# Kernel tuning notes

Measured on AMD Instinct MI355X. Metric: run time of the kernel, lower is better.

Reference implementation:

```python
import jax, jax.numpy as jnp
import numpy as np

IN_F, OUT_F, MAX_LEN = 768, 512, 1024
NEG_INF = -9e15

def leaky_relu(x, slope=0.2):
    return jnp.where(x >= 0, x, slope * x)

def setup_inputs() -> dict:
    key = jax.random.key(0)
    k1, k2, k3, k4, k5, k6, k7 = jax.random.split(key, 7)
    B, N = 8, 1024
    h = jax.random.normal(k1, (B, N, IN_F), dtype=jnp.float32)
    adj = jax.random.randint(k2, (B, N, N), 0, 2, dtype=jnp.int32)
    positions = jax.random.randint(k3, (B, N), 0, MAX_LEN, dtype=jnp.int64)
    # learned params (nn.Linear stores weight [out,in]; we keep [in,out] for x@W)
    W = jax.random.normal(k4, (IN_F, OUT_F), dtype=jnp.float32) / np.sqrt(IN_F)
    # a: Linear(2*OUT_F, 1) -> vector of length 2*OUT_F, split into a1 (self) / a2 (neighbor)
    a = jax.random.normal(k5, (2 * OUT_F,), dtype=jnp.float32) / np.sqrt(2 * OUT_F)
    pos_table = jax.random.normal(k6, (MAX_LEN, OUT_F), dtype=jnp.float32) * 0.02
    return {"h": h, "adj": adj, "positions": positions, "W": W, "a": a, "pos_table": pos_table}

def reference(h, adj, positions, W, a, pos_table):
    # Wh: [B,N,Do]
    Wh = jnp.einsum("bnd,do->bno", h, W) + pos_table[positions]
    # additive-attention trick: a([Wh_i ; Wh_j]) = Wh_i@a1 + Wh_j@a2
    a1, a2 = a[:OUT_F], a[OUT_F:]
    f1 = Wh @ a1  # [B,N] score contribution of source (repeat_interleave side)
    f2 = Wh @ a2  # [B,N] score contribution of target (repeat side)
    e = leaky_relu(f1[:, :, None] + f2[:, None, :])  # [B,N,N]
    e = jnp.where(adj > 0, e, NEG_INF)
    attention = jax.nn.softmax(e, axis=-1)  # [B,N,N]
    h_prime = jnp.einsum("bnm,bmo->bno", attention, Wh)  # [B,N,Do]
    return h_prime, attention
```

## Files before the change

### kernel.cpp

```cpp
#include <hip/hip_runtime.h>
#include <stdint.h>

#define BATCH 8
#define NNODE 1024
#define INF 768
#define OUTF 512
#define MTOT (BATCH * NNODE)

typedef __attribute__((ext_vector_type(8))) short short8;
typedef __attribute__((ext_vector_type(4))) short short4v;
typedef __attribute__((ext_vector_type(4))) float floatx4;

__device__ __forceinline__ unsigned short f2bf(float f) {
  union { float f; unsigned u; } v; v.f = f;
  unsigned r = v.u + 0x7fffu + ((v.u >> 16) & 1u);
  return (unsigned short)(r >> 16);
}

__device__ __forceinline__ void gload_lds16(const void* g, void* l) {
  __builtin_amdgcn_global_load_lds(
      (const __attribute__((address_space(1))) void*)g,
      (__attribute__((address_space(3))) void*)l, 16, 0, 0);
}

__global__ __launch_bounds__(256) void prep_kernel(
    const float* __restrict__ h, const float* __restrict__ W,
    short* __restrict__ hbf, short* __restrict__ Wt, float* __restrict__ f12) {
  __shared__ float tile[32][33];
  int bid = blockIdx.x;
  int t = threadIdx.x;
  if (bid < 3072) {
    size_t i = ((size_t)bid * 256 + t) * 8;
    float4 v0 = *(const float4*)&h[i];
    float4 v1 = *(const float4*)&h[i + 4];
    short8 o;
    o[0] = (short)f2bf(v0.x); o[1] = (short)f2bf(v0.y);
    o[2] = (short)f2bf(v0.z); o[3] = (short)f2bf(v0.w);
    o[4] = (short)f2bf(v1.x); o[5] = (short)f2bf(v1.y);
    o[6] = (short)f2bf(v1.z); o[7] = (short)f2bf(v1.w);
    *(short8*)&hbf[i] = o;
    if (bid < 16) {
      float4 z = make_float4(0.f, 0.f, 0.f, 0.f);
      *(float4*)&f12[bid * 1024 + t * 4] = z;
    }
  } else {
    int tb = bid - 3072;
    int o0 = (tb & 15) * 32;
    int k0 = (tb >> 4) * 32;
    int x = t & 31, y = t >> 5;
#pragma unroll
    for (int q = 0; q < 4; ++q) {
      int r = y * 4 + q;
      tile[r][x] = W[(size_t)(k0 + r) * OUTF + o0 + x];
    }
    __syncthreads();
#pragma unroll
    for (int q = 0; q < 4; ++q) {
      int r = y * 4 + q;
      Wt[(size_t)(o0 + r) * INF + k0 + x] = (short)f2bf(tile[x][r]);
    }
  }
}

__global__ __launch_bounds__(512) void gemm1_kernel(
    const short* __restrict__ hbf, const short* __restrict__ Wt,
    const int* __restrict__ positions, const float* __restrict__ pos_table,
    const float* __restrict__ a, float* __restrict__ f12,
    short* __restrict__ Wht) {
  __shared__ short smem[4][8192];
  int bid0 = blockIdx.x;
  int bid = (bid0 & 7) * 32 + (bid0 >> 3);
  int nt = bid & 3, mt = bid >> 2;
  int M0 = mt * 128, N0 = nt * 128;
  int t = threadIdx.x;
  int wv = t >> 6, lane = t & 63;
  int wr = (wv >> 2) * 64, wc = (wv & 3) * 32;
  int l16 = lane & 15, kq = lane >> 4;

  floatx4 acc[4][2] = {};

  auto stage = [&](int buf, int kt) {
#pragma unroll
    for (int i = 0; i < 2; ++i) {
      int q = wv * 64 + lane + i * 512;
      int row = q >> 3;
      int cg = (q & 7) ^ (row & 7);
      gload_lds16(&hbf[(size_t)(M0 + row) * INF + kt * 64 + cg * 8],
                  &smem[buf * 2][(wv * 64 + i * 512) * 8]);
      gload_lds16(&Wt[(size_t)(N0 + row) * INF + kt * 64 + cg * 8],
                  &smem[buf * 2 + 1][(wv * 64 + i * 512) * 8]);
    }
  };

  stage(0, 0);
  __syncthreads();
  int cur = 0;
  for (int kt = 0; kt < 12; ++kt) {
    if (kt < 11) stage(cur ^ 1, kt + 1);
    const short* As = smem[cur * 2];
    const short* Bs = smem[cur * 2 + 1];
#pragma unroll
    for (int ks = 0; ks < 2; ++ks) {
      short8 af[4], bfv[2];
#pragma unroll
      for (int mi = 0; mi < 4; ++mi) {
        int r = wr + mi * 16 + l16;
        af[mi] = *(const short8*)&As[r * 64 + (((ks * 4 + kq) ^ (r & 7)) * 8)];
      }
#pragma unroll
      for (int ni = 0; ni < 2; ++ni) {
        int r = wc + ni * 16 + l16;
        bfv[ni] = *(const short8*)&Bs[r * 64 + (((ks * 4 + kq) ^ (r & 7)) * 8)];
      }
#pragma unroll
      for (int mi = 0; mi < 4; ++mi)
#pragma unroll
        for (int ni = 0; ni < 2; ++ni)
          acc[mi][ni] = __builtin_amdgcn_mfma_f32_16x16x32_bf16(af[mi], bfv[ni], acc[mi][ni], 0, 0, 0);
    }
    __syncthreads();
    cur ^= 1;
  }

  int oc0 = N0 + wc + l16;
  int oc1 = oc0 + 16;
#pragma unroll
  for (int mi = 0; mi < 4; ++mi)
#pragma unroll
    for (int j = 0; j < 4; ++j) {
      int row = M0 + wr + mi * 16 + kq * 4 + j;
      int pos = positions[row];
      acc[mi][0][j] += pos_table[(size_t)pos * OUTF + oc0];
      acc[mi][1][j] += pos_table[(size_t)pos * OUTF + oc1];
    }
  short* T = &smem[0][0];
#pragma unroll
  for (int mi = 0; mi < 4; ++mi)
#pragma unroll
    for (int ni = 0; ni < 2; ++ni)
#pragma unroll
      for (int j = 0; j < 4; ++j)
        T[(wc + ni * 16 + l16) * 136 + wr + mi * 16 + kq * 4 + j] =
            (short)f2bf(acc[mi][ni][j]);
  float a10 = a[oc0], a11 = a[oc1];
  float a20 = a[OUTF + oc0], a21 = a[OUTF + oc1];
  float v1[16], v2[16];
#pragma unroll
  for (int mi = 0; mi < 4; ++mi)
#pragma unroll
    for (int j = 0; j < 4; ++j) {
      v1[mi * 4 + j] = acc[mi][0][j] * a10 + acc[mi][1][j] * a11;
      v2[mi * 4 + j] = acc[mi][0][j] * a20 + acc[mi][1][j] * a21;
    }
#pragma unroll
  for (int mlen = 8; mlen >= 1; mlen >>= 1) {
    bool hi = (l16 & mlen) != 0;
#pragma unroll
    for (int i = 0; i < mlen; ++i) {
      float k1 = hi ? v1[mlen + i] : v1[i];
      float s1 = hi ? v1[i] : v1[mlen + i];
      float k2 = hi ? v2[mlen + i] : v2[i];
      float s2 = hi ? v2[i] : v2[mlen + i];
      v1[i] = k1 + __shfl_xor(s1, mlen);
      v2[i] = k2 + __shfl_xor(s2, mlen);
    }
  }
  {
    int rrow = M0 + wr + (l16 >> 2) * 16 + kq * 4 + (l16 & 3);
    atomicAdd(&f12[rrow], v1[0]);
    atomicAdd(&f12[MTOT + rrow], v2[0]);
  }
  __syncthreads();
  int bb = M0 >> 10, i0 = M0 & 1023;
#pragma unroll
  for (int i = 0; i < 4; ++i) {
    int c = t + i * 512;
    int row = c >> 4;
    int mc = (c & 15) * 8;
    short8 vv = *(const short8*)&T[row * 136 + mc];
    *(short8*)&Wht[((size_t)bb * OUTF + N0 + row) * NNODE + i0 + mc] = vv;
  }
}

__global__ __launch_bounds__(256) void softmax_kernel(
    const float* __restrict__ f1, const float* __restrict__ f2,
    const int* __restrict__ adj, float* __restrict__ att,
    short* __restrict__ attbf) {
  int m = blockIdx.x;
  int b = m >> 10;
  int t = threadIdx.x;
  int wave = t >> 6, lane = t & 63;
  __shared__ float red[4];
  float f1v = f1[m];
  int4 av = ((const int4*)(adj + (size_t)m * NNODE))[t];
  float4 fv = ((const float4*)(f2 + b * NNODE))[t];
  float e[4];
  {
    float x;
    x = f1v + fv.x; x = x >= 0.f ? x : 0.2f * x; e[0] = av.x > 0 ? x : -9e15f;
    x = f1v + fv.y; x = x >= 0.f ? x : 0.2f * x; e[1] = av.y > 0 ? x : -9e15f;
    x = f1v + fv.z; x = x >= 0.f ? x : 0.2f * x; e[2] = av.z > 0 ? x : -9e15f;
    x = f1v + fv.w; x = x >= 0.f ? x : 0.2f * x; e[3] = av.w > 0 ? x : -9e15f;
  }
  float mx = fmaxf(fmaxf(e[0], e[1]), fmaxf(e[2], e[3]));
#pragma unroll
  for (int off = 32; off; off >>= 1) mx = fmaxf(mx, __shfl_xor(mx, off));
  if (lane == 0) red[wave] = mx;
  __syncthreads();
  mx = fmaxf(fmaxf(red[0], red[1]), fmaxf(red[2], red[3]));
  __syncthreads();
  float p[4], s = 0.f;
#pragma unroll
  for (int q = 0; q < 4; ++q) { p[q] = expf(e[q] - mx); s += p[q]; }
#pragma unroll
  for (int off = 32; off; off >>= 1) s += __shfl_xor(s, off);
  if (lane == 0) red[wave] = s;
  __syncthreads();
  s = red[0] + red[1] + red[2] + red[3];
  float inv = 1.f / s;
  float4 o = make_float4(p[0] * inv, p[1] * inv, p[2] * inv, p[3] * inv);
  ((float4*)(att + (size_t)m * NNODE))[t] = o;
  short4v ob;
  ob[0] = (short)f2bf(o.x); ob[1] = (short)f2bf(o.y);
  ob[2] = (short)f2bf(o.z); ob[3] = (short)f2bf(o.w);
  ((short4v*)(attbf + (size_t)m * NNODE))[t] = ob;
}

__global__ __launch_bounds__(512) void pv_kernel(
    const short* __restrict__ attbf, const short* __restrict__ Wht,
    float* __restrict__ hp) {
  __shared__ short smem[4][8192];
  int bid0 = blockIdx.x;
  int bid = (bid0 & 7) * 32 + (bid0 >> 3);
  int nt = bid & 3, mt = bid >> 2;
  int M0 = mt * 128, N0 = nt * 128;
  const short* Wb = Wht + (size_t)(M0 >> 10) * OUTF * NNODE;
  int t = threadIdx.x;
  int wv = t >> 6, lane = t & 63;
  int wr = (wv >> 2) * 64, wc = (wv & 3) * 32;
  int l16 = lane & 15, kq = lane >> 4;

  floatx4 acc[4][2] = {};

  auto stage = [&](int buf, int kt) {
#pragma unroll
    for (int i = 0; i < 2; ++i) {
      int q = wv * 64 + lane + i * 512;
      int row = q >> 3;
      int cg = (q & 7) ^ (row & 7);
      gload_lds16(&attbf[(size_t)(M0 + row) * NNODE + kt * 64 + cg * 8],
                  &smem[buf * 2][(wv * 64 + i * 512) * 8]);
      gload_lds16(&Wb[(size_t)(N0 + row) * NNODE + kt * 64 + cg * 8],
                  &smem[buf * 2 + 1][(wv * 64 + i * 512) * 8]);
    }
  };

  stage(0, 0);
  __syncthreads();
  int cur = 0;
  for (int kt = 0; kt < 16; ++kt) {
    if (kt < 15) stage(cur ^ 1, kt + 1);
    const short* As = smem[cur * 2];
    const short* Bs = smem[cur * 2 + 1];
#pragma unroll
    for (int ks = 0; ks < 2; ++ks) {
      short8 af[4], bfv[2];
#pragma unroll
      for (int mi = 0; mi < 4; ++mi) {
        int r = wr + mi * 16 + l16;
        af[mi] = *(const short8*)&As[r * 64 + (((ks * 4 + kq) ^ (r & 7)) * 8)];
      }
#pragma unroll
      for (int ni = 0; ni < 2; ++ni) {
        int r = wc + ni * 16 + l16;
        bfv[ni] = *(const short8*)&Bs[r * 64 + (((ks * 4 + kq) ^ (r & 7)) * 8)];
      }
#pragma unroll
      for (int mi = 0; mi < 4; ++mi)
#pragma unroll
        for (int ni = 0; ni < 2; ++ni)
          acc[mi][ni] = __builtin_amdgcn_mfma_f32_16x16x32_bf16(af[mi], bfv[ni], acc[mi][ni], 0, 0, 0);
    }
    __syncthreads();
    cur ^= 1;
  }

#pragma unroll
  for (int mi = 0; mi < 4; ++mi) {
#pragma unroll
    for (int j = 0; j < 4; ++j) {
      int row = M0 + wr + mi * 16 + kq * 4 + j;
#pragma unroll
      for (int ni = 0; ni < 2; ++ni) {
        int col = N0 + wc + ni * 16 + l16;
        hp[(size_t)row * OUTF + col] = acc[mi][ni][j];
      }
    }
  }
}

extern "C" void kernel_launch(void* const* d_in, const int* in_sizes, int n_in,
                              void* d_out, int out_size, void* d_ws, size_t ws_size,
                              hipStream_t stream) {
  const float* h = (const float*)d_in[0];
  const int* adj = (const int*)d_in[1];
  const int* positions = (const int*)d_in[2];
  const float* W = (const float*)d_in[3];
  const float* a = (const float*)d_in[4];
  const float* pos_table = (const float*)d_in[5];

  float* hp = (float*)d_out;
  float* att = hp + (size_t)MTOT * OUTF;

  char* ws = (char*)d_ws;
  short* Wt = (short*)ws;
  short* Wht = (short*)(ws + 786432);
  float* f12 = (float*)(ws + 786432 + 8388608);
  short* hbf = (short*)(ws + 786432 + 8388608 + 65536);
  short* attbf = hbf;

  prep_kernel<<<3456, 256, 0, stream>>>(h, W, hbf, Wt, f12);
  gemm1_kernel<<<256, 512, 0, stream>>>(hbf, Wt, positions, pos_table, a, f12, Wht);
  softmax_kernel<<<8192, 256, 0, stream>>>(f12, f12 + MTOT, adj, att, attbf);
  pv_kernel<<<256, 512, 0, stream>>>(attbf, Wht, hp);
}
```

Measured before the change: 58.40 us.

## Fuse masked softmax into PV GEMM, keeping bf16 probabilities in LDS

Replaces the separate softmax and PV kernels with one kernel. Each block computes the masked leaky-relu softmax for 32 rows across all 1024 columns, writes the fp32 attention output, and stores the bf16 probabilities in swizzled LDS. It then multiplies them by the full 512-wide Wh tile streamed through double-buffered LDS. This removes the bf16 attention round-trip through global memory and one launch. The cost is only 256 blocks, each holding 64 exp values per thread in registers, and a full pass over Wh per 32 rows.

```diff
diff --git a/kernel.cpp b/kernel.cpp
--- a/kernel.cpp
+++ b/kernel.cpp
@@ -182,121 +182,115 @@
   }
 }
 
-__global__ __launch_bounds__(256) void softmax_kernel(
-    const float* __restrict__ f1, const float* __restrict__ f2,
-    const int* __restrict__ adj, float* __restrict__ att,
-    short* __restrict__ attbf) {
-  int m = blockIdx.x;
-  int b = m >> 10;
-  int t = threadIdx.x;
-  int wave = t >> 6, lane = t & 63;
-  __shared__ float red[4];
-  float f1v = f1[m];
-  int4 av = ((const int4*)(adj + (size_t)m * NNODE))[t];
-  float4 fv = ((const float4*)(f2 + b * NNODE))[t];
-  float e[4];
-  {
-    float x;
-    x = f1v + fv.x; x = x >= 0.f ? x : 0.2f * x; e[0] = av.x > 0 ? x : -9e15f;
-    x = f1v + fv.y; x = x >= 0.f ? x : 0.2f * x; e[1] = av.y > 0 ? x : -9e15f;
-    x = f1v + fv.z; x = x >= 0.f ? x : 0.2f * x; e[2] = av.z > 0 ? x : -9e15f;
-    x = f1v + fv.w; x = x >= 0.f ? x : 0.2f * x; e[3] = av.w > 0 ? x : -9e15f;
-  }
-  float mx = fmaxf(fmaxf(e[0], e[1]), fmaxf(e[2], e[3]));
-#pragma unroll
-  for (int off = 32; off; off >>= 1) mx = fmaxf(mx, __shfl_xor(mx, off));
-  if (lane == 0) red[wave] = mx;
-  __syncthreads();
-  mx = fmaxf(fmaxf(red[0], red[1]), fmaxf(red[2], red[3]));
-  __syncthreads();
-  float p[4], s = 0.f;
-#pragma unroll
-  for (int q = 0; q < 4; ++q) { p[q] = expf(e[q] - mx); s += p[q]; }
-#pragma unroll
-  for (int off = 32; off; off >>= 1) s += __shfl_xor(s, off);
-  if (lane == 0) red[wave] = s;
-  __syncthreads();
-  s = red[0] + red[1] + red[2] + red[3];
-  float inv = 1.f / s;
-  float4 o = make_float4(p[0] * inv, p[1] * inv, p[2] * inv, p[3] * inv);
-  ((float4*)(att + (size_t)m * NNODE))[t] = o;
-  short4v ob;
-  ob[0] = (short)f2bf(o.x); ob[1] = (short)f2bf(o.y);
-  ob[2] = (short)f2bf(o.z); ob[3] = (short)f2bf(o.w);
-  ((short4v*)(attbf + (size_t)m * NNODE))[t] = ob;
-}
-
-__global__ __launch_bounds__(512) void pv_kernel(
-    const short* __restrict__ attbf, const short* __restrict__ Wht,
+__global__ __launch_bounds__(512) void smpv_kernel(
+    const float* __restrict__ f12, const int* __restrict__ adj,
+    const short* __restrict__ Wht, float* __restrict__ att,
     float* __restrict__ hp) {
-  __shared__ short smem[4][8192];
+  __shared__ short lds[65536];
+  short* pbf = lds;
+  short* Bbuf0 = lds + 32768;
+  short* Bbuf1 = lds + 49152;
+
   int bid0 = blockIdx.x;
-  int bid = (bid0 & 7) * 32 + (bid0 >> 3);
-  int nt = bid & 3, mt = bid >> 2;
-  int M0 = mt * 128, N0 = nt * 128;
-  const short* Wb = Wht + (size_t)(M0 >> 10) * OUTF * NNODE;
+  int b = bid0 & 7, rb = bid0 >> 3;
+  int r0 = rb * 32;
   int t = threadIdx.x;
   int wv = t >> 6, lane = t & 63;
-  int wr = (wv >> 2) * 64, wc = (wv & 3) * 32;
   int l16 = lane & 15, kq = lane >> 4;
-
-  floatx4 acc[4][2] = {};
-
-  auto stage = [&](int buf, int kt) {
-#pragma unroll
-    for (int i = 0; i < 2; ++i) {
+  const short* Wb = Wht + (size_t)b * OUTF * NNODE;
+
+  auto stageB = [&](short* dst, int kt) {
+#pragma unroll
+    for (int i = 0; i < 4; ++i) {
       int q = wv * 64 + lane + i * 512;
-      int row = q >> 3;
-      int cg = (q & 7) ^ (row & 7);
-      gload_lds16(&attbf[(size_t)(M0 + row) * NNODE + kt * 64 + cg * 8],
-                  &smem[buf * 2][(wv * 64 + i * 512) * 8]);
-      gload_lds16(&Wb[(size_t)(N0 + row) * NNODE + kt * 64 + cg * 8],
-                  &smem[buf * 2 + 1][(wv * 64 + i * 512) * 8]);
+      int r = q >> 2, s = q & 3;
+      int cg = s ^ (r & 3);
+      gload_lds16(&Wb[(size_t)r * NNODE + kt * 32 + cg * 8],
+                  dst + (wv * 64 + i * 512) * 8);
     }
   };
-
-  stage(0, 0);
+  stageB(Bbuf0, 0);
+
+  {
+    int row = t >> 4, sub = t & 15;
+    int gm = b * NNODE + r0 + row;
+    float f1v = f12[gm];
+    const float* f2b = f12 + MTOT + b * NNODE;
+    const int* adjrow = adj + (size_t)gm * NNODE;
+    float e[64];
+#pragma unroll
+    for (int i = 0; i < 16; ++i) {
+      int col = sub * 4 + i * 64;
+      int4 av = *(const int4*)&adjrow[col];
+      float4 fv = *(const float4*)&f2b[col];
+      float x;
+      x = f1v + fv.x; x = x >= 0.f ? x : 0.2f * x; e[i * 4 + 0] = av.x > 0 ? x : -9e15f;
+      x = f1v + fv.y; x = x >= 0.f ? x : 0.2f * x; e[i * 4 + 1] = av.y > 0 ? x : -9e15f;
+      x = f1v + fv.z; x = x >= 0.f ? x : 0.2f * x; e[i * 4 + 2] = av.z > 0 ? x : -9e15f;
+      x = f1v + fv.w; x = x >= 0.f ? x : 0.2f * x; e[i * 4 + 3] = av.w > 0 ? x : -9e15f;
+    }
+    float mx = e[0];
+#pragma unroll
+    for (int i = 1; i < 64; ++i) mx = fmaxf(mx, e[i]);
+#pragma unroll
+    for (int off = 1; off < 16; off <<= 1) mx = fmaxf(mx, __shfl_xor(mx, off));
+    float s = 0.f;
+#pragma unroll
+    for (int i = 0; i < 64; ++i) { e[i] = expf(e[i] - mx); s += e[i]; }
+#pragma unroll
+    for (int off = 1; off < 16; off <<= 1) s += __shfl_xor(s, off);
+    float inv = 1.f / s;
+    float* attrow = att + (size_t)gm * NNODE;
+#pragma unroll
+    for (int i = 0; i < 16; ++i) {
+      int col = sub * 4 + i * 64;
+      float4 o = make_float4(e[i * 4] * inv, e[i * 4 + 1] * inv,
+                             e[i * 4 + 2] * inv, e[i * 4 + 3] * inv);
+      *(float4*)&attrow[col] = o;
+      int c = (sub >> 1) + 8 * i;
+      short4v pb;
+      pb[0] = (short)f2bf(o.x); pb[1] = (short)f2bf(o.y);
+      pb[2] = (short)f2bf(o.z); pb[3] = (short)f2bf(o.w);
+      *(short4v*)&pbf[row * 1024 + ((c ^ (row & 7)) * 8) + (sub & 1) * 4] = pb;
+    }
+  }
   __syncthreads();
+
+  int wc = wv * 64;
+  floatx4 acc[2][4] = {};
   int cur = 0;
-  for (int kt = 0; kt < 16; ++kt) {
-    if (kt < 15) stage(cur ^ 1, kt + 1);
-    const short* As = smem[cur * 2];
-    const short* Bs = smem[cur * 2 + 1];
-#pragma unroll
-    for (int ks = 0; ks < 2; ++ks) {
-      short8 af[4], bfv[2];
-#pragma unroll
-      for (int mi = 0; mi < 4; ++mi) {
-        int r = wr + mi * 16 + l16;
-        af[mi] = *(const short8*)&As[r * 64 + (((ks * 4 + kq) ^ (r & 7)) * 8)];
-      }
-#pragma unroll
-      for (int ni = 0; ni < 2; ++ni) {
-        int r = wc + ni * 16 + l16;
-        bfv[ni] = *(const short8*)&Bs[r * 64 + (((ks * 4 + kq) ^ (r & 7)) * 8)];
-      }
-#pragma unroll
-      for (int mi = 0; mi < 4; ++mi)
-#pragma unroll
-        for (int ni = 0; ni < 2; ++ni)
-          acc[mi][ni] = __builtin_amdgcn_mfma_f32_16x16x32_bf16(af[mi], bfv[ni], acc[mi][ni], 0, 0, 0);
-    }
+  for (int kt = 0; kt < 32; ++kt) {
+    if (kt < 31) stageB(cur ? Bbuf0 : Bbuf1, kt + 1);
+    const short* Bsc = cur ? Bbuf1 : Bbuf0;
+    short8 af[2], bfv[4];
+#pragma unroll
+    for (int mi = 0; mi < 2; ++mi) {
+      int r = mi * 16 + l16;
+      af[mi] = *(const short8*)&pbf[r * 1024 + (((kt * 4 + kq) ^ (r & 7)) * 8)];
+    }
+#pragma unroll
+    for (int ni = 0; ni < 4; ++ni) {
+      int r = wc + ni * 16 + l16;
+      bfv[ni] = *(const short8*)&Bsc[r * 32 + ((kq ^ (r & 3)) * 8)];
+    }
+#pragma unroll
+    for (int mi = 0; mi < 2; ++mi)
+#pragma unroll
+      for (int ni = 0; ni < 4; ++ni)
+        acc[mi][ni] = __builtin_amdgcn_mfma_f32_16x16x32_bf16(af[mi], bfv[ni], acc[mi][ni], 0, 0, 0);
     __syncthreads();
     cur ^= 1;
   }
 
 #pragma unroll
-  for (int mi = 0; mi < 4; ++mi) {
+  for (int mi = 0; mi < 2; ++mi)
 #pragma unroll
     for (int j = 0; j < 4; ++j) {
-      int row = M0 + wr + mi * 16 + kq * 4 + j;
-#pragma unroll
-      for (int ni = 0; ni < 2; ++ni) {
-        int col = N0 + wc + ni * 16 + l16;
-        hp[(size_t)row * OUTF + col] = acc[mi][ni][j];
-      }
-    }
-  }
+      int grow = b * NNODE + r0 + mi * 16 + kq * 4 + j;
+#pragma unroll
+      for (int ni = 0; ni < 4; ++ni)
+        hp[(size_t)grow * OUTF + wc + ni * 16 + l16] = acc[mi][ni][j];
+    }
 }
 
 extern "C" void kernel_launch(void* const* d_in, const int* in_sizes, int n_in,
@@ -317,10 +311,8 @@
   short* Wht = (short*)(ws + 786432);
   float* f12 = (float*)(ws + 786432 + 8388608);
   short* hbf = (short*)(ws + 786432 + 8388608 + 65536);
-  short* attbf = hbf;
 
   prep_kernel<<<3456, 256, 0, stream>>>(h, W, hbf, Wt, f12);
   gemm1_kernel<<<256, 512, 0, stream>>>(hbf, Wt, positions, pos_table, a, f12, Wht);
-  softmax_kernel<<<8192, 256, 0, stream>>>(f12, f12 + MTOT, adj, att, attbf);
-  pv_kernel<<<256, 512, 0, stream>>>(attbf, Wht, hp);
-}
+  smpv_kernel<<<256, 512, 0, stream>>>(f12, adj, Wht, att, hp);
+}
```

Measured after the change: 68.54 us. +17.4%, slower.

## Use 4-wave 64x64 warp tiles with K-tile 32 in both GEMM kernels

Applied to the files above, without the earlier changes.

Both MFMA GEMM kernels drop from 512 to 256 threads per block. Each wave now computes a 64x64 output tile instead of 64x32, and the LDS K-tile shrinks from 64 to 32 with a matching XOR swizzle. This raises fragment reuse per wave and lowers LDS footprint. The cost is half the waves per CU for latency hiding and twice as many K iterations and barriers.

```diff
diff --git a/kernel.cpp b/kernel.cpp
--- a/kernel.cpp
+++ b/kernel.cpp
@@ -62,95 +62,98 @@
   }
 }
 
-__global__ __launch_bounds__(512) void gemm1_kernel(
+__global__ __launch_bounds__(256) void gemm1_kernel(
     const short* __restrict__ hbf, const short* __restrict__ Wt,
     const int* __restrict__ positions, const float* __restrict__ pos_table,
     const float* __restrict__ a, float* __restrict__ f12,
     short* __restrict__ Wht) {
-  __shared__ short smem[4][8192];
+  __shared__ short smem[20480];
   int bid0 = blockIdx.x;
   int bid = (bid0 & 7) * 32 + (bid0 >> 3);
   int nt = bid & 3, mt = bid >> 2;
   int M0 = mt * 128, N0 = nt * 128;
   int t = threadIdx.x;
   int wv = t >> 6, lane = t & 63;
-  int wr = (wv >> 2) * 64, wc = (wv & 3) * 32;
+  int wr = (wv >> 1) * 64, wc = (wv & 1) * 64;
   int l16 = lane & 15, kq = lane >> 4;
 
-  floatx4 acc[4][2] = {};
+  floatx4 acc[4][4] = {};
 
   auto stage = [&](int buf, int kt) {
 #pragma unroll
     for (int i = 0; i < 2; ++i) {
-      int q = wv * 64 + lane + i * 512;
-      int row = q >> 3;
-      int cg = (q & 7) ^ (row & 7);
-      gload_lds16(&hbf[(size_t)(M0 + row) * INF + kt * 64 + cg * 8],
-                  &smem[buf * 2][(wv * 64 + i * 512) * 8]);
-      gload_lds16(&Wt[(size_t)(N0 + row) * INF + kt * 64 + cg * 8],
-                  &smem[buf * 2 + 1][(wv * 64 + i * 512) * 8]);
+      int q = t + i * 256;
+      int row = q >> 2;
+      int cg = (q & 3) ^ ((row >> 1) & 3);
+      gload_lds16(&hbf[(size_t)(M0 + row) * INF + kt * 32 + cg * 8],
+                  &smem[buf * 4096 + q * 8]);
+      gload_lds16(&Wt[(size_t)(N0 + row) * INF + kt * 32 + cg * 8],
+                  &smem[8192 + buf * 4096 + q * 8]);
     }
   };
 
   stage(0, 0);
   __syncthreads();
-  int cur = 0;
-  for (int kt = 0; kt < 12; ++kt) {
-    if (kt < 11) stage(cur ^ 1, kt + 1);
-    const short* As = smem[cur * 2];
-    const short* Bs = smem[cur * 2 + 1];
-#pragma unroll
-    for (int ks = 0; ks < 2; ++ks) {
-      short8 af[4], bfv[2];
-#pragma unroll
-      for (int mi = 0; mi < 4; ++mi) {
-        int r = wr + mi * 16 + l16;
-        af[mi] = *(const short8*)&As[r * 64 + (((ks * 4 + kq) ^ (r & 7)) * 8)];
-      }
-#pragma unroll
-      for (int ni = 0; ni < 2; ++ni) {
-        int r = wc + ni * 16 + l16;
-        bfv[ni] = *(const short8*)&Bs[r * 64 + (((ks * 4 + kq) ^ (r & 7)) * 8)];
-      }
-#pragma unroll
-      for (int mi = 0; mi < 4; ++mi)
-#pragma unroll
-        for (int ni = 0; ni < 2; ++ni)
-          acc[mi][ni] = __builtin_amdgcn_mfma_f32_16x16x32_bf16(af[mi], bfv[ni], acc[mi][ni], 0, 0, 0);
-    }
+  for (int kt = 0; kt < 24; ++kt) {
+    if (kt < 23) stage((kt + 1) & 1, kt + 1);
+    const short* As = &smem[(kt & 1) * 4096];
+    const short* Bs = &smem[8192 + (kt & 1) * 4096];
+    short8 af[4], bfv[4];
+#pragma unroll
+    for (int mi = 0; mi < 4; ++mi) {
+      int r = wr + mi * 16 + l16;
+      af[mi] = *(const short8*)&As[r * 32 + ((kq ^ ((r >> 1) & 3)) * 8)];
+    }
+#pragma unroll
+    for (int ni = 0; ni < 4; ++ni) {
+      int r = wc + ni * 16 + l16;
+      bfv[ni] = *(const short8*)&Bs[r * 32 + ((kq ^ ((r >> 1) & 3)) * 8)];
+    }
+#pragma unroll
+    for (int mi = 0; mi < 4; ++mi)
+#pragma unroll
+      for (int ni = 0; ni < 4; ++ni)
+        acc[mi][ni] = __builtin_amdgcn_mfma_f32_16x16x32_bf16(af[mi], bfv[ni], acc[mi][ni], 0, 0, 0);
     __syncthreads();
-    cur ^= 1;
-  }
-
-  int oc0 = N0 + wc + l16;
-  int oc1 = oc0 + 16;
+  }
+
+  int oc[4];
+#pragma unroll
+  for (int ni = 0; ni < 4; ++ni) oc[ni] = N0 + wc + ni * 16 + l16;
 #pragma unroll
   for (int mi = 0; mi < 4; ++mi)
 #pragma unroll
     for (int j = 0; j < 4; ++j) {
       int row = M0 + wr + mi * 16 + kq * 4 + j;
       int pos = positions[row];
-      acc[mi][0][j] += pos_table[(size_t)pos * OUTF + oc0];
-      acc[mi][1][j] += pos_table[(size_t)pos * OUTF + oc1];
-    }
-  short* T = &smem[0][0];
+      const float* pt = &pos_table[(size_t)pos * OUTF];
+#pragma unroll
+      for (int ni = 0; ni < 4; ++ni) acc[mi][ni][j] += pt[oc[ni]];
+    }
+  short* T = smem;
 #pragma unroll
   for (int mi = 0; mi < 4; ++mi)
 #pragma unroll
-    for (int ni = 0; ni < 2; ++ni)
+    for (int ni = 0; ni < 4; ++ni)
 #pragma unroll
       for (int j = 0; j < 4; ++j)
         T[(wc + ni * 16 + l16) * 136 + wr + mi * 16 + kq * 4 + j] =
             (short)f2bf(acc[mi][ni][j]);
-  float a10 = a[oc0], a11 = a[oc1];
-  float a20 = a[OUTF + oc0], a21 = a[OUTF + oc1];
+  float a1v[4], a2v[4];
+#pragma unroll
+  for (int ni = 0; ni < 4; ++ni) { a1v[ni] = a[oc[ni]]; a2v[ni] = a[OUTF + oc[ni]]; }
   float v1[16], v2[16];
 #pragma unroll
   for (int mi = 0; mi < 4; ++mi)
 #pragma unroll
     for (int j = 0; j < 4; ++j) {
-      v1[mi * 4 + j] = acc[mi][0][j] * a10 + acc[mi][1][j] * a11;
-      v2[mi * 4 + j] = acc[mi][0][j] * a20 + acc[mi][1][j] * a21;
+      float s1 = 0.f, s2 = 0.f;
+#pragma unroll
+      for (int ni = 0; ni < 4; ++ni) {
+        s1 += acc[mi][ni][j] * a1v[ni];
+        s2 += acc[mi][ni][j] * a2v[ni];
+      }
+      v1[mi * 4 + j] = s1; v2[mi * 4 + j] = s2;
     }
 #pragma unroll
   for (int mlen = 8; mlen >= 1; mlen >>= 1) {
@@ -173,8 +176,8 @@
   __syncthreads();
   int bb = M0 >> 10, i0 = M0 & 1023;
 #pragma unroll
-  for (int i = 0; i < 4; ++i) {
-    int c = t + i * 512;
+  for (int i = 0; i < 8; ++i) {
+    int c = t + i * 256;
     int row = c >> 4;
     int mc = (c & 15) * 8;
     short8 vv = *(const short8*)&T[row * 136 + mc];
@@ -226,10 +229,10 @@
   ((short4v*)(attbf + (size_t)m * NNODE))[t] = ob;
 }
 
-__global__ __launch_bounds__(512) void pv_kernel(
+__global__ __launch_bounds__(256) void pv_kernel(
     const short* __restrict__ attbf, const short* __restrict__ Wht,
     float* __restrict__ hp) {
-  __shared__ short smem[4][8192];
+  __shared__ short smem[16384];
   int bid0 = blockIdx.x;
   int bid = (bid0 & 7) * 32 + (bid0 >> 3);
   int nt = bid & 3, mt = bid >> 2;
@@ -237,66 +240,58 @@
   const short* Wb = Wht + (size_t)(M0 >> 10) * OUTF * NNODE;
   int t = threadIdx.x;
   int wv = t >> 6, lane = t & 63;
-  int wr = (wv >> 2) * 64, wc = (wv & 3) * 32;
+  int wr = (wv >> 1) * 64, wc = (wv & 1) * 64;
   int l16 = lane & 15, kq = lane >> 4;
 
-  floatx4 acc[4][2] = {};
+  floatx4 acc[4][4] = {};
 
   auto stage = [&](int buf, int kt) {
 #pragma unroll
     for (int i = 0; i < 2; ++i) {
-      int q = wv * 64 + lane + i * 512;
-      int row = q >> 3;
-      int cg = (q & 7) ^ (row & 7);
-      gload_lds16(&attbf[(size_t)(M0 + row) * NNODE + kt * 64 + cg * 8],
-                  &smem[buf * 2][(wv * 64 + i * 512) * 8]);
-      gload_lds16(&Wb[(size_t)(N0 + row) * NNODE + kt * 64 + cg * 8],
-                  &smem[buf * 2 + 1][(wv * 64 + i * 512) * 8]);
+      int q = t + i * 256;
+      int row = q >> 2;
+      int cg = (q & 3) ^ ((row >> 1) & 3);
+      gload_lds16(&attbf[(size_t)(M0 + row) * NNODE + kt * 32 + cg * 8],
+                  &smem[buf * 4096 + q * 8]);
+      gload_lds16(&Wb[(size_t)(N0 + row) * NNODE + kt * 32 + cg * 8],
+                  &smem[8192 + buf * 4096 + q * 8]);
     }
   };
 
   stage(0, 0);
   __syncthreads();
-  int cur = 0;
-  for (int kt = 0; kt < 16; ++kt) {
-    if (kt < 15) stage(cur ^ 1, kt + 1);
-    const short* As = smem[cur * 2];
-    const short* Bs = smem[cur * 2 + 1];
-#pragma unroll
-    for (int ks = 0; ks < 2; ++ks) {
-      short8 af[4], bfv[2];
-#pragma unroll
-      for (int mi = 0; mi < 4; ++mi) {
-        int r = wr + mi * 16 + l16;
-        af[mi] = *(const short8*)&As[r * 64 + (((ks * 4 + kq) ^ (r & 7)) * 8)];
-      }
-#pragma unroll
-      for (int ni = 0; ni < 2; ++ni) {
-        int r = wc + ni * 16 + l16;
-        bfv[ni] = *(const short8*)&Bs[r * 64 + (((ks * 4 + kq) ^ (r & 7)) * 8)];
-      }
-#pragma unroll
-      for (int mi = 0; mi < 4; ++mi)
-#pragma unroll
-        for (int ni = 0; ni < 2; ++ni)
-          acc[mi][ni] = __builtin_amdgcn_mfma_f32_16x16x32_bf16(af[mi], bfv[ni], acc[mi][ni], 0, 0, 0);
-    }
+  for (int kt = 0; kt < 32; ++kt) {
+    if (kt < 31) stage((kt + 1) & 1, kt + 1);
+    const short* As = &smem[(kt & 1) * 4096];
+    const short* Bs = &smem[8192 + (kt & 1) * 4096];
+    short8 af[4], bfv[4];
+#pragma unroll
+    for (int mi = 0; mi < 4; ++mi) {
+      int r = wr + mi * 16 + l16;
+      af[mi] = *(const short8*)&As[r * 32 + ((kq ^ ((r >> 1) & 3)) * 8)];
+    }
+#pragma unroll
+    for (int ni = 0; ni < 4; ++ni) {
+      int r = wc + ni * 16 + l16;
+      bfv[ni] = *(const short8*)&Bs[r * 32 + ((kq ^ ((r >> 1) & 3)) * 8)];
+    }
+#pragma unroll
+    for (int mi = 0; mi < 4; ++mi)
+#pragma unroll
+      for (int ni = 0; ni < 4; ++ni)
+        acc[mi][ni] = __builtin_amdgcn_mfma_f32_16x16x32_bf16(af[mi], bfv[ni], acc[mi][ni], 0, 0, 0);
     __syncthreads();
-    cur ^= 1;
-  }
-
-#pragma unroll
-  for (int mi = 0; mi < 4; ++mi) {
+  }
+
+#pragma unroll
+  for (int mi = 0; mi < 4; ++mi)
 #pragma unroll
     for (int j = 0; j < 4; ++j) {
       int row = M0 + wr + mi * 16 + kq * 4 + j;
 #pragma unroll
-      for (int ni = 0; ni < 2; ++ni) {
-        int col = N0 + wc + ni * 16 + l16;
-        hp[(size_t)row * OUTF + col] = acc[mi][ni][j];
-      }
-    }
-  }
+      for (int ni = 0; ni < 4; ++ni)
+        hp[(size_t)row * OUTF + N0 + wc + ni * 16 + l16] = acc[mi][ni][j];
+    }
 }
 
 extern "C" void kernel_launch(void* const* d_in, const int* in_sizes, int n_in,
@@ -320,7 +315,7 @@
   short* attbf = hbf;
 
   prep_kernel<<<3456, 256, 0, stream>>>(h, W, hbf, Wt, f12);
-  gemm1_kernel<<<256, 512, 0, stream>>>(hbf, Wt, positions, pos_table, a, f12, Wht);
+  gemm1_kernel<<<256, 256, 0, stream>>>(hbf, Wt, positions, pos_table, a, f12, Wht);
   softmax_kernel<<<8192, 256, 0, stream>>>(f12, f12 + MTOT, adj, att, attbf);
-  pv_kernel<<<256, 512, 0, stream>>>(attbf, Wht, hp);
-}
+  pv_kernel<<<256, 256, 0, stream>>>(attbf, Wht, hp);
+}
```

New measurement: 68.76 us. +17.7%, slower.

## Fuse fp32-to-bf16 conversion of h and attention into GEMM A-tile loads

Applied to the files above, without the earlier changes.

Removes the separate bf16 copies of h (built in prep_kernel) and of the attention matrix (written by softmax). Both GEMMs now load the fp32 A operand into registers, convert to bf16, and store it swizzled into LDS, with the load for the next k-tile issued before the MFMAs. This avoids writing and rereading the bf16 intermediates in global memory. In exchange each GEMM reads twice as many A bytes, and loses the async global_load_lds path for A, so more registers and VALU work are used.

```diff
diff --git a/kernel.cpp b/kernel.cpp
--- a/kernel.cpp
+++ b/kernel.cpp
@@ -24,29 +24,14 @@
 }
 
 __global__ __launch_bounds__(256) void prep_kernel(
-    const float* __restrict__ h, const float* __restrict__ W,
-    short* __restrict__ hbf, short* __restrict__ Wt, float* __restrict__ f12) {
+    const float* __restrict__ W, short* __restrict__ Wt,
+    float* __restrict__ f12) {
   __shared__ float tile[32][33];
   int bid = blockIdx.x;
   int t = threadIdx.x;
-  if (bid < 3072) {
-    size_t i = ((size_t)bid * 256 + t) * 8;
-    float4 v0 = *(const float4*)&h[i];
-    float4 v1 = *(const float4*)&h[i + 4];
-    short8 o;
-    o[0] = (short)f2bf(v0.x); o[1] = (short)f2bf(v0.y);
-    o[2] = (short)f2bf(v0.z); o[3] = (short)f2bf(v0.w);
-    o[4] = (short)f2bf(v1.x); o[5] = (short)f2bf(v1.y);
-    o[6] = (short)f2bf(v1.z); o[7] = (short)f2bf(v1.w);
-    *(short8*)&hbf[i] = o;
-    if (bid < 16) {
-      float4 z = make_float4(0.f, 0.f, 0.f, 0.f);
-      *(float4*)&f12[bid * 1024 + t * 4] = z;
-    }
-  } else {
-    int tb = bid - 3072;
-    int o0 = (tb & 15) * 32;
-    int k0 = (tb >> 4) * 32;
+  if (bid < 384) {
+    int o0 = (bid & 15) * 32;
+    int k0 = (bid >> 4) * 32;
     int x = t & 31, y = t >> 5;
 #pragma unroll
     for (int q = 0; q < 4; ++q) {
@@ -59,11 +44,15 @@
       int r = y * 4 + q;
       Wt[(size_t)(o0 + r) * INF + k0 + x] = (short)f2bf(tile[x][r]);
     }
+  } else {
+    int z = bid - 384;
+    float4 zz = make_float4(0.f, 0.f, 0.f, 0.f);
+    *(float4*)&f12[z * 1024 + t * 4] = zz;
   }
 }
 
 __global__ __launch_bounds__(512) void gemm1_kernel(
-    const short* __restrict__ hbf, const short* __restrict__ Wt,
+    const float* __restrict__ h, const short* __restrict__ Wt,
     const int* __restrict__ positions, const float* __restrict__ pos_table,
     const float* __restrict__ a, float* __restrict__ f12,
     short* __restrict__ Wht) {
@@ -76,27 +65,50 @@
   int wv = t >> 6, lane = t & 63;
   int wr = (wv >> 2) * 64, wc = (wv & 3) * 32;
   int l16 = lane & 15, kq = lane >> 4;
+  int arow0 = t >> 3, ac = t & 7;
 
   floatx4 acc[4][2] = {};
-
-  auto stage = [&](int buf, int kt) {
+  float4 areg[4];
+
+  auto aload = [&](int kt) {
+#pragma unroll
+    for (int i = 0; i < 2; ++i) {
+      const float* src = &h[(size_t)(M0 + arow0 + i * 64) * INF + kt * 64 + ac * 8];
+      areg[i * 2] = *(const float4*)src;
+      areg[i * 2 + 1] = *(const float4*)(src + 4);
+    }
+  };
+  auto awrite = [&](int buf) {
+#pragma unroll
+    for (int i = 0; i < 2; ++i) {
+      int row = arow0 + i * 64;
+      short8 o;
+      o[0] = (short)f2bf(areg[i * 2].x); o[1] = (short)f2bf(areg[i * 2].y);
+      o[2] = (short)f2bf(areg[i * 2].z); o[3] = (short)f2bf(areg[i * 2].w);
+      o[4] = (short)f2bf(areg[i * 2 + 1].x); o[5] = (short)f2bf(areg[i * 2 + 1].y);
+      o[6] = (short)f2bf(areg[i * 2 + 1].z); o[7] = (short)f2bf(areg[i * 2 + 1].w);
+      *(short8*)&smem[buf * 2][row * 64 + ((ac ^ (row & 7)) * 8)] = o;
+    }
+  };
+  auto stageB = [&](int buf, int kt) {
 #pragma unroll
     for (int i = 0; i < 2; ++i) {
       int q = wv * 64 + lane + i * 512;
       int row = q >> 3;
       int cg = (q & 7) ^ (row & 7);
-      gload_lds16(&hbf[(size_t)(M0 + row) * INF + kt * 64 + cg * 8],
-                  &smem[buf * 2][(wv * 64 + i * 512) * 8]);
       gload_lds16(&Wt[(size_t)(N0 + row) * INF + kt * 64 + cg * 8],
                   &smem[buf * 2 + 1][(wv * 64 + i * 512) * 8]);
     }
   };
 
-  stage(0, 0);
-  __syncthreads();
-  int cur = 0;
+  aload(0);
+  stageB(0, 0);
+  awrite(0);
+  __syncthreads();
+
   for (int kt = 0; kt < 12; ++kt) {
-    if (kt < 11) stage(cur ^ 1, kt + 1);
+    int cur = kt & 1, nxt = cur ^ 1;
+    if (kt < 11) { aload(kt + 1); stageB(nxt, kt + 1); }
     const short* As = smem[cur * 2];
     const short* Bs = smem[cur * 2 + 1];
 #pragma unroll
@@ -118,8 +130,8 @@
         for (int ni = 0; ni < 2; ++ni)
           acc[mi][ni] = __builtin_amdgcn_mfma_f32_16x16x32_bf16(af[mi], bfv[ni], acc[mi][ni], 0, 0, 0);
     }
+    if (kt < 11) awrite(nxt);
     __syncthreads();
-    cur ^= 1;
   }
 
   int oc0 = N0 + wc + l16;
@@ -184,8 +196,7 @@
 
 __global__ __launch_bounds__(256) void softmax_kernel(
     const float* __restrict__ f1, const float* __restrict__ f2,
-    const int* __restrict__ adj, float* __restrict__ att,
-    short* __restrict__ attbf) {
+    const int* __restrict__ adj, float* __restrict__ att) {
   int m = blockIdx.x;
   int b = m >> 10;
   int t = threadIdx.x;
@@ -220,14 +231,10 @@
   float inv = 1.f / s;
   float4 o = make_float4(p[0] * inv, p[1] * inv, p[2] * inv, p[3] * inv);
   ((float4*)(att + (size_t)m * NNODE))[t] = o;
-  short4v ob;
-  ob[0] = (short)f2bf(o.x); ob[1] = (short)f2bf(o.y);
-  ob[2] = (short)f2bf(o.z); ob[3] = (short)f2bf(o.w);
-  ((short4v*)(attbf + (size_t)m * NNODE))[t] = ob;
 }
 
 __global__ __launch_bounds__(512) void pv_kernel(
-    const short* __restrict__ attbf, const short* __restrict__ Wht,
+    const float* __restrict__ att, const short* __restrict__ Wht,
     float* __restrict__ hp) {
   __shared__ short smem[4][8192];
   int bid0 = blockIdx.x;
@@ -239,27 +246,50 @@
   int wv = t >> 6, lane = t & 63;
   int wr = (wv >> 2) * 64, wc = (wv & 3) * 32;
   int l16 = lane & 15, kq = lane >> 4;
+  int arow0 = t >> 3, ac = t & 7;
 
   floatx4 acc[4][2] = {};
-
-  auto stage = [&](int buf, int kt) {
+  float4 areg[4];
+
+  auto aload = [&](int kt) {
+#pragma unroll
+    for (int i = 0; i < 2; ++i) {
+      const float* src = &att[(size_t)(M0 + arow0 + i * 64) * NNODE + kt * 64 + ac * 8];
+      areg[i * 2] = *(const float4*)src;
+      areg[i * 2 + 1] = *(const float4*)(src + 4);
+    }
+  };
+  auto awrite = [&](int buf) {
+#pragma unroll
+    for (int i = 0; i < 2; ++i) {
+      int row = arow0 + i * 64;
+      short8 o;
+      o[0] = (short)f2bf(areg[i * 2].x); o[1] = (short)f2bf(areg[i * 2].y);
+      o[2] = (short)f2bf(areg[i * 2].z); o[3] = (short)f2bf(areg[i * 2].w);
+      o[4] = (short)f2bf(areg[i * 2 + 1].x); o[5] = (short)f2bf(areg[i * 2 + 1].y);
+      o[6] = (short)f2bf(areg[i * 2 + 1].z); o[7] = (short)f2bf(areg[i * 2 + 1].w);
+      *(short8*)&smem[buf * 2][row * 64 + ((ac ^ (row & 7)) * 8)] = o;
+    }
+  };
+  auto stageB = [&](int buf, int kt) {
 #pragma unroll
     for (int i = 0; i < 2; ++i) {
       int q = wv * 64 + lane + i * 512;
       int row = q >> 3;
       int cg = (q & 7) ^ (row & 7);
-      gload_lds16(&attbf[(size_t)(M0 + row) * NNODE + kt * 64 + cg * 8],
-                  &smem[buf * 2][(wv * 64 + i * 512) * 8]);
       gload_lds16(&Wb[(size_t)(N0 + row) * NNODE + kt * 64 + cg * 8],
                   &smem[buf * 2 + 1][(wv * 64 + i * 512) * 8]);
     }
   };
 
-  stage(0, 0);
-  __syncthreads();
-  int cur = 0;
+  aload(0);
+  stageB(0, 0);
+  awrite(0);
+  __syncthreads();
+
   for (int kt = 0; kt < 16; ++kt) {
-    if (kt < 15) stage(cur ^ 1, kt + 1);
+    int cur = kt & 1, nxt = cur ^ 1;
+    if (kt < 15) { aload(kt + 1); stageB(nxt, kt + 1); }
     const short* As = smem[cur * 2];
     const short* Bs = smem[cur * 2 + 1];
 #pragma unroll
@@ -281,12 +311,12 @@
         for (int ni = 0; ni < 2; ++ni)
           acc[mi][ni] = __builtin_amdgcn_mfma_f32_16x16x32_bf16(af[mi], bfv[ni], acc[mi][ni], 0, 0, 0);
     }
+    if (kt < 15) awrite(nxt);
     __syncthreads();
-    cur ^= 1;
-  }
-
-#pragma unroll
-  for (int mi = 0; mi < 4; ++mi) {
+  }
+
+#pragma unroll
+  for (int mi = 0; mi < 4; ++mi)
 #pragma unroll
     for (int j = 0; j < 4; ++j) {
       int row = M0 + wr + mi * 16 + kq * 4 + j;
@@ -296,7 +326,6 @@
         hp[(size_t)row * OUTF + col] = acc[mi][ni][j];
       }
     }
-  }
 }
 
 extern "C" void kernel_launch(void* const* d_in, const int* in_sizes, int n_in,
@@ -316,11 +345,9 @@
   short* Wt = (short*)ws;
   short* Wht = (short*)(ws + 786432);
   float* f12 = (float*)(ws + 786432 + 8388608);
-  short* hbf = (short*)(ws + 786432 + 8388608 + 65536);
-  short* attbf = hbf;
-
-  prep_kernel<<<3456, 256, 0, stream>>>(h, W, hbf, Wt, f12);
-  gemm1_kernel<<<256, 512, 0, stream>>>(hbf, Wt, positions, pos_table, a, f12, Wht);
-  softmax_kernel<<<8192, 256, 0, stream>>>(f12, f12 + MTOT, adj, att, attbf);
-  pv_kernel<<<256, 512, 0, stream>>>(attbf, Wht, hp);
-}
+
+  prep_kernel<<<400, 256, 0, stream>>>(W, Wt, f12);
+  gemm1_kernel<<<256, 512, 0, stream>>>(h, Wt, positions, pos_table, a, f12, Wht);
+  softmax_kernel<<<8192, 256, 0, stream>>>(f12, f12 + MTOT, adj, att);
+  pv_kernel<<<256, 512, 0, stream>>>(att, Wht, hp);
+}
```

New measurement: 64.96 us. +11.2%, slower.
